# Optimization experiments

Hardware: AMD Instinct MI355X
Metric: run time of the kernel (lower is better)

The kernel has to match this reference:

```python
import jax, jax.numpy as jnp
import numpy as np

BATCH, DIM = 8192, 1024  # batch of ODE states, state dimension (orig dim=100 scaled up)
ETA = 1.0                # self.eta
B_DECAY = 1.0            # self.B (linear decay coefficient)


def setup_inputs() -> dict:
    key = jax.random.key(0)
    k1, k2, k3, k4, k5 = jax.random.split(key, 5)
    return {
        "x":      jax.random.normal(k1, (BATCH, DIM), jnp.float32),
        "e_x":    jax.random.normal(k2, (BATCH, DIM), jnp.float32),
        "W":      jax.random.normal(k3, (BATCH, DIM), jnp.float32),
        "A":      jax.random.normal(k4, (DIM, DIM), jnpp := jnp.float32) / np.float32(np.sqrt(DIM)),
        "target": jax.random.normal(k5, (1, DIM), jnp.float32),
    }


def reference(x, e_x, W, A, target):
    # b_ast = diagonal of B_ast = diag(target^2 / (1 + target^2)); mm with a diag
    # matrix == elementwise multiply by its diagonal.  [1, D]
    b_ast = target ** 2 / (1.0 + target ** 2)
    # control: u = -eta * (W * (x + e_x - target)) @ B_ast              [B, D]
    u = -ETA * (W * ((x + e_x) - target)) * b_ast
    # saturating nonlinearity sigma(x) = x^2 / (1 + x^2)                [B, D]
    sig = x ** 2 / (1.0 + x ** 2)
    # dx = -B*x + A @ sigma(x) (per state: sigma(x) @ A^T) + u*sigma(x) [B, D]
    dx = -B_DECAY * x + sig @ A.T + u * sig
    # original returns tuple(dx_i) + tuple(-dx_i) + tuple(zeros): stack as [3, B, D]
    return jnp.stack([dx, -dx, jnp.zeros_like(dx)])
```

## Files before the change

kernel.cpp:

```cpp
#include <hip/hip_runtime.h>
#include <hip/hip_bf16.h>
#include <stdint.h>

#define BATCH 8192
#define DIM   1024
#define BM 128
#define BN 64
#define BK 64
#define STEPS 16
#define BUF 24576

typedef __attribute__((ext_vector_type(4))) float f32x4;
typedef __attribute__((ext_vector_type(8))) short bf16x8;
typedef __attribute__((ext_vector_type(8))) unsigned short u16x8;

#define AS1(p) ((const __attribute__((address_space(1))) void*)(p))
#define AS3(p) ((__attribute__((address_space(3))) void*)(p))

__device__ __forceinline__ unsigned short f2bf(float f) {
    union { __hip_bfloat16 h; unsigned short u; } v;
    v.h = __hip_bfloat16(f);
    return v.u;
}
__device__ __forceinline__ float sigma_f(float x) {
    float x2 = x * x;
    return x2 * __builtin_amdgcn_rcpf(1.0f + x2);
}

__global__ __launch_bounds__(256) void prep_kernel(
    const float* __restrict__ x, const float* __restrict__ A,
    unsigned short* __restrict__ sigb, unsigned short* __restrict__ Abf)
{
    const int i = blockIdx.x * 256 + threadIdx.x;
    if (i < BATCH * DIM / 8) {
        f32x4 v0 = ((const f32x4*)x)[i * 2];
        f32x4 v1 = ((const f32x4*)x)[i * 2 + 1];
        u16x8 sb;
#pragma unroll
        for (int e = 0; e < 4; ++e) {
            sb[e]     = f2bf(sigma_f(v0[e]));
            sb[e + 4] = f2bf(sigma_f(v1[e]));
        }
        ((u16x8*)sigb)[i] = sb;
    } else {
        const int j = i - BATCH * DIM / 8;
        f32x4 v0 = ((const f32x4*)A)[j * 2];
        f32x4 v1 = ((const f32x4*)A)[j * 2 + 1];
        u16x8 ab;
#pragma unroll
        for (int e = 0; e < 4; ++e) {
            ab[e]     = f2bf(v0[e]);
            ab[e + 4] = f2bf(v1[e]);
        }
        ((u16x8*)Abf)[j] = ab;
    }
}

__global__ __launch_bounds__(256, 2) void gemm_kernel(
    const float* __restrict__ x, const float* __restrict__ ex,
    const float* __restrict__ W, const float* __restrict__ tgt,
    const unsigned short* __restrict__ sigb,
    const unsigned short* __restrict__ Abf,
    float* __restrict__ out0, float* __restrict__ out1,
    float* __restrict__ out2)
{
    __shared__ __align__(16) char lds[3 * BUF];

    const int b     = blockIdx.x;
    const int xcd   = b & 7;
    const int local = b >> 3;
    const int bm    = xcd * 8 + (local >> 4);
    const int bn    = local & 15;

    const int tid  = threadIdx.x;
    const int lane = tid & 63;
    const int wid  = tid >> 6;
    const int wr   = wid >> 1, wc = wid & 1;
    const int l15  = lane & 15;

    const int swz = (((lane & 7) ^ (lane >> 3)) << 4);
    const char* gS = (const char*)sigb +
        ((size_t)(bm * BM + wid * 8 + (lane >> 3)) * DIM) * 2 + swz;
    const char* gB = (const char*)Abf +
        ((size_t)(bn * BN + wid * 8 + (lane >> 3)) * DIM) * 2 + swz;

    const int rd_sw = (lane & 7) << 4;
    const int cb0   = (lane >> 4) << 4;

    f32x4 acc[4][2];
#pragma unroll
    for (int mi = 0; mi < 4; ++mi)
#pragma unroll
        for (int ni = 0; ni < 2; ++ni)
            acc[mi][ni] = f32x4{0.f, 0.f, 0.f, 0.f};

    auto stage = [&](int t) {
        char* As = lds + (t % 3) * BUF;
        char* Bs = As + 16384;
        const size_t ko = (size_t)t * (BK * 2);
#pragma unroll
        for (int j = 0; j < 4; ++j)
            __builtin_amdgcn_global_load_lds(
                AS1(gS + (size_t)j * (32 * DIM * 2) + ko),
                AS3(As + (wid * 8 + j * 32) * 128), 16, 0, 0);
#pragma unroll
        for (int j = 0; j < 2; ++j)
            __builtin_amdgcn_global_load_lds(
                AS1(gB + (size_t)j * (32 * DIM * 2) + ko),
                AS3(Bs + (wid * 8 + j * 32) * 128), 16, 0, 0);
    };

    stage(0);
    stage(1);

    for (int t = 0; t < STEPS; ++t) {
        __builtin_amdgcn_sched_barrier(0);
        if (t < STEPS - 1) asm volatile("s_waitcnt vmcnt(6)" ::: "memory");
        else               asm volatile("s_waitcnt vmcnt(0)" ::: "memory");
        __builtin_amdgcn_sched_barrier(0);
        __builtin_amdgcn_s_barrier();
        __builtin_amdgcn_sched_barrier(0);
        if (t + 2 < STEPS) stage(t + 2);
        __builtin_amdgcn_sched_barrier(0);

        const char* As_ = lds + (t % 3) * BUF;
        const char* Bs_ = As_ + 16384;
#pragma unroll
        for (int kk = 0; kk < 2; ++kk) {
            bf16x8 af[4], bfr[2];
#pragma unroll
            for (int mi = 0; mi < 4; ++mi)
                af[mi] = *(const bf16x8*)(As_ + (wr * 64 + mi * 16 + l15) * 128 +
                                          ((cb0 + kk * 64) ^ rd_sw));
#pragma unroll
            for (int ni = 0; ni < 2; ++ni)
                bfr[ni] = *(const bf16x8*)(Bs_ + (wc * 32 + ni * 16 + l15) * 128 +
                                           ((cb0 + kk * 64) ^ rd_sw));
#pragma unroll
            for (int mi = 0; mi < 4; ++mi)
#pragma unroll
                for (int ni = 0; ni < 2; ++ni)
                    acc[mi][ni] = __builtin_amdgcn_mfma_f32_16x16x32_bf16(
                        af[mi], bfr[ni], acc[mi][ni], 0, 0, 0);
        }
    }

    __syncthreads();
#pragma unroll
    for (int mi = 0; mi < 4; ++mi)
#pragma unroll
        for (int ni = 0; ni < 2; ++ni) {
            const int row_ = wr * 64 + mi * 16 + ((lane >> 4) << 2);
            const int colb = (wc * 32 + ni * 16 + l15) * 4;
#pragma unroll
            for (int r = 0; r < 4; ++r)
                *(float*)(lds + (row_ + r) * 256 + colb) = acc[mi][ni][r];
        }
    __syncthreads();

#pragma unroll
    for (int p = 0; p < 8; ++p) {
        const int ci  = p * 256 + tid;
        const int row = ci >> 4;
        const int cv  = ci & 15;
        f32x4 c = *(const f32x4*)(lds + row * 256 + cv * 16);
        const size_t v4 = (size_t)(bm * BM + row) * (DIM / 4) + bn * 16 + cv;
        f32x4 xv = ((const f32x4*)x)[v4];
        f32x4 ev = ((const f32x4*)ex)[v4];
        f32x4 wv = ((const f32x4*)W)[v4];
        f32x4 tv = ((const f32x4*)tgt)[bn * 16 + cv];
        f32x4 o0;
#pragma unroll
        for (int e = 0; e < 4; ++e) {
            float xi = xv[e], ti = tv[e];
            float ba = ti * ti * __builtin_amdgcn_rcpf(1.0f + ti * ti);
            float u  = -(wv[e] * (xi + ev[e] - ti)) * ba;
            float s  = sigma_f(xi);
            o0[e] = -xi + u * s + c[e];
        }
        ((f32x4*)out0)[v4] = o0;
        ((f32x4*)out1)[v4] = -o0;
        ((f32x4*)out2)[v4] = f32x4{0.f, 0.f, 0.f, 0.f};
    }
}

extern "C" void kernel_launch(void* const* d_in, const int* in_sizes, int n_in,
                              void* d_out, int out_size, void* d_ws, size_t ws_size,
                              hipStream_t stream)
{
    const float* x   = (const float*)d_in[0];
    const float* ex  = (const float*)d_in[1];
    const float* W   = (const float*)d_in[2];
    const float* A   = (const float*)d_in[3];
    const float* tgt = (const float*)d_in[4];

    float* out0 = (float*)d_out;
    float* out1 = out0 + (size_t)BATCH * DIM;
    float* out2 = out1 + (size_t)BATCH * DIM;

    unsigned short* sigb = (unsigned short*)d_ws;
    unsigned short* Abf  = (unsigned short*)((char*)d_ws + (size_t)16 * 1024 * 1024);

    prep_kernel<<<4608, 256, 0, stream>>>(x, A, sigb, Abf);
    gemm_kernel<<<(BATCH / BM) * (DIM / BN), 256, 0, stream>>>(
        x, ex, W, tgt, sigb, Abf, out0, out1, out2);
}
```

Measured before the change: 55.71 us.

## Fuse sigma and bf16 conversion of x into GEMM A-operand load

Removes the separate pass that computes sigma(x) in bf16 into workspace. The GEMM now streams fp32 x tiles straight into LDS and applies sigma plus the bf16 conversion while reading MFMA fragments. The M tile is halved to 64 so the fp32 tile fits the LDS buffers, which doubles the grid and means each block re-reads the A operand more often. Each x element is now loaded and converted by all 16 column blocks instead of once, and fp32 x traffic to LDS doubles compared with the bf16 staging.

```diff
diff --git a/kernel.cpp b/kernel.cpp
--- a/kernel.cpp
+++ b/kernel.cpp
@@ -4,7 +4,7 @@
 
 #define BATCH 8192
 #define DIM   1024
-#define BM 128
+#define BM 64
 #define BN 64
 #define BK 64
 #define STEPS 16
@@ -27,39 +27,24 @@
     return x2 * __builtin_amdgcn_rcpf(1.0f + x2);
 }
 
-__global__ __launch_bounds__(256) void prep_kernel(
-    const float* __restrict__ x, const float* __restrict__ A,
-    unsigned short* __restrict__ sigb, unsigned short* __restrict__ Abf)
+__global__ __launch_bounds__(256) void convA_kernel(
+    const float* __restrict__ A, unsigned short* __restrict__ Ab)
 {
     const int i = blockIdx.x * 256 + threadIdx.x;
-    if (i < BATCH * DIM / 8) {
-        f32x4 v0 = ((const f32x4*)x)[i * 2];
-        f32x4 v1 = ((const f32x4*)x)[i * 2 + 1];
-        u16x8 sb;
-#pragma unroll
-        for (int e = 0; e < 4; ++e) {
-            sb[e]     = f2bf(sigma_f(v0[e]));
-            sb[e + 4] = f2bf(sigma_f(v1[e]));
-        }
-        ((u16x8*)sigb)[i] = sb;
-    } else {
-        const int j = i - BATCH * DIM / 8;
-        f32x4 v0 = ((const f32x4*)A)[j * 2];
-        f32x4 v1 = ((const f32x4*)A)[j * 2 + 1];
-        u16x8 ab;
-#pragma unroll
-        for (int e = 0; e < 4; ++e) {
-            ab[e]     = f2bf(v0[e]);
-            ab[e + 4] = f2bf(v1[e]);
-        }
-        ((u16x8*)Abf)[j] = ab;
+    f32x4 v0 = ((const f32x4*)A)[i * 2];
+    f32x4 v1 = ((const f32x4*)A)[i * 2 + 1];
+    u16x8 ab;
+#pragma unroll
+    for (int e = 0; e < 4; ++e) {
+        ab[e]     = f2bf(v0[e]);
+        ab[e + 4] = f2bf(v1[e]);
     }
+    ((u16x8*)Ab)[i] = ab;
 }
 
 __global__ __launch_bounds__(256, 2) void gemm_kernel(
     const float* __restrict__ x, const float* __restrict__ ex,
     const float* __restrict__ W, const float* __restrict__ tgt,
-    const unsigned short* __restrict__ sigb,
     const unsigned short* __restrict__ Abf,
     float* __restrict__ out0, float* __restrict__ out1,
     float* __restrict__ out2)
@@ -69,7 +54,7 @@
     const int b     = blockIdx.x;
     const int xcd   = b & 7;
     const int local = b >> 3;
-    const int bm    = xcd * 8 + (local >> 4);
+    const int bm    = xcd * 16 + (local >> 4);
     const int bn    = local & 15;
 
     const int tid  = threadIdx.x;
@@ -78,36 +63,41 @@
     const int wr   = wid >> 1, wc = wid & 1;
     const int l15  = lane & 15;
 
-    const int swz = (((lane & 7) ^ (lane >> 3)) << 4);
-    const char* gS = (const char*)sigb +
-        ((size_t)(bm * BM + wid * 8 + (lane >> 3)) * DIM) * 2 + swz;
+    const char* xB = (const char*)x + (size_t)(bm * BM) * (DIM * 4);
+
+    const int swzB = (((lane & 7) ^ (lane >> 3)) << 4);
     const char* gB = (const char*)Abf +
-        ((size_t)(bn * BN + wid * 8 + (lane >> 3)) * DIM) * 2 + swz;
+        ((size_t)(bn * BN + wid * 16 + (lane >> 3)) * DIM) * 2 + swzB;
+
+    const int xrow_base = wid * 16 + (lane >> 4);
 
     const int rd_sw = (lane & 7) << 4;
     const int cb0   = (lane >> 4) << 4;
-
-    f32x4 acc[4][2];
-#pragma unroll
-    for (int mi = 0; mi < 4; ++mi)
+    const int kbA   = (lane >> 4) << 5;
+
+    f32x4 acc[2][2];
+#pragma unroll
+    for (int mi = 0; mi < 2; ++mi)
 #pragma unroll
         for (int ni = 0; ni < 2; ++ni)
             acc[mi][ni] = f32x4{0.f, 0.f, 0.f, 0.f};
 
     auto stage = [&](int t) {
-        char* As = lds + (t % 3) * BUF;
-        char* Bs = As + 16384;
-        const size_t ko = (size_t)t * (BK * 2);
-#pragma unroll
-        for (int j = 0; j < 4; ++j)
+        char* Xs = lds + (t % 3) * BUF;
+        char* Bs = Xs + 16384;
+#pragma unroll
+        for (int j = 0; j < 4; ++j) {
+            const int row = xrow_base + j * 4;
             __builtin_amdgcn_global_load_lds(
-                AS1(gS + (size_t)j * (32 * DIM * 2) + ko),
-                AS3(As + (wid * 8 + j * 32) * 128), 16, 0, 0);
+                AS1(xB + (size_t)row * (DIM * 4) + (size_t)t * 256 +
+                    (((l15) * 16) ^ ((row & 7) << 4))),
+                AS3(Xs + (wid * 16 + j * 4) * 256), 16, 0, 0);
+        }
 #pragma unroll
         for (int j = 0; j < 2; ++j)
             __builtin_amdgcn_global_load_lds(
-                AS1(gB + (size_t)j * (32 * DIM * 2) + ko),
-                AS3(Bs + (wid * 8 + j * 32) * 128), 16, 0, 0);
+                AS1(gB + (size_t)j * (8 * DIM * 2) + (size_t)t * 128),
+                AS3(Bs + (wid * 16 + j * 8) * 128), 16, 0, 0);
     };
 
     stage(0);
@@ -123,21 +113,31 @@
         if (t + 2 < STEPS) stage(t + 2);
         __builtin_amdgcn_sched_barrier(0);
 
-        const char* As_ = lds + (t % 3) * BUF;
-        const char* Bs_ = As_ + 16384;
+        const char* Xs_ = lds + (t % 3) * BUF;
+        const char* Bs_ = Xs_ + 16384;
 #pragma unroll
         for (int kk = 0; kk < 2; ++kk) {
-            bf16x8 af[4], bfr[2];
-#pragma unroll
-            for (int mi = 0; mi < 4; ++mi)
-                af[mi] = *(const bf16x8*)(As_ + (wr * 64 + mi * 16 + l15) * 128 +
-                                          ((cb0 + kk * 64) ^ rd_sw));
+            bf16x8 af[2], bfr[2];
+#pragma unroll
+            for (int mi = 0; mi < 2; ++mi) {
+                const int arow = wr * 32 + mi * 16 + l15;
+                const int kb   = kk * 128 + kbA;
+                f32x4 f0 = *(const f32x4*)(Xs_ + arow * 256 + (kb ^ rd_sw));
+                f32x4 f1 = *(const f32x4*)(Xs_ + arow * 256 + ((kb + 16) ^ rd_sw));
+                union { u16x8 u; bf16x8 bv; } cvu;
+#pragma unroll
+                for (int i = 0; i < 4; ++i) {
+                    cvu.u[i]     = f2bf(sigma_f(f0[i]));
+                    cvu.u[i + 4] = f2bf(sigma_f(f1[i]));
+                }
+                af[mi] = cvu.bv;
+            }
 #pragma unroll
             for (int ni = 0; ni < 2; ++ni)
                 bfr[ni] = *(const bf16x8*)(Bs_ + (wc * 32 + ni * 16 + l15) * 128 +
                                            ((cb0 + kk * 64) ^ rd_sw));
 #pragma unroll
-            for (int mi = 0; mi < 4; ++mi)
+            for (int mi = 0; mi < 2; ++mi)
 #pragma unroll
                 for (int ni = 0; ni < 2; ++ni)
                     acc[mi][ni] = __builtin_amdgcn_mfma_f32_16x16x32_bf16(
@@ -147,10 +147,10 @@
 
     __syncthreads();
 #pragma unroll
-    for (int mi = 0; mi < 4; ++mi)
+    for (int mi = 0; mi < 2; ++mi)
 #pragma unroll
         for (int ni = 0; ni < 2; ++ni) {
-            const int row_ = wr * 64 + mi * 16 + ((lane >> 4) << 2);
+            const int row_ = wr * 32 + mi * 16 + ((lane >> 4) << 2);
             const int colb = (wc * 32 + ni * 16 + l15) * 4;
 #pragma unroll
             for (int r = 0; r < 4; ++r)
@@ -159,7 +159,7 @@
     __syncthreads();
 
 #pragma unroll
-    for (int p = 0; p < 8; ++p) {
+    for (int p = 0; p < 4; ++p) {
         const int ci  = p * 256 + tid;
         const int row = ci >> 4;
         const int cv  = ci & 15;
@@ -198,10 +198,9 @@
     float* out1 = out0 + (size_t)BATCH * DIM;
     float* out2 = out1 + (size_t)BATCH * DIM;
 
-    unsigned short* sigb = (unsigned short*)d_ws;
-    unsigned short* Abf  = (unsigned short*)((char*)d_ws + (size_t)16 * 1024 * 1024);
-
-    prep_kernel<<<4608, 256, 0, stream>>>(x, A, sigb, Abf);
+    unsigned short* Abf = (unsigned short*)d_ws;
+
+    convA_kernel<<<DIM * DIM / 8 / 256, 256, 0, stream>>>(A, Abf);
     gemm_kernel<<<(BATCH / BM) * (DIM / BN), 256, 0, stream>>>(
-        x, ex, W, tgt, sigb, Abf, out0, out1, out2);
-}
+        x, ex, W, tgt, Abf, out0, out1, out2);
+}
```

New measurement: 81.19 us. 45.7% more time.
